# Optimization experiments

Hardware: AMD Instinct MI355X
Metric: run time of the kernel (lower is better)

## Reference

```python
import jax, jax.numpy as jnp
import numpy as np

N_NODES = 100000
N_EDGES = 1200000
D_FEAT = 64


def setup_inputs() -> dict:
    key = jax.random.key(0)
    k1, k2, k3 = jax.random.split(key, 3)
    x = jax.random.normal(k1, (N_NODES, D_FEAT), dtype=jnp.float32)
    edge_index = jax.random.randint(k2, (2, N_EDGES), 0, N_NODES, dtype=jnp.int64)
    edge_weight = jax.random.uniform(k3, (N_EDGES, 1), dtype=jnp.float32)
    return {"x": x, "edge_index": edge_index, "edge_weight": edge_weight}


def reference(x, edge_index, edge_weight):
    # flow = source_to_target: j = edge_index[0] (source), i = edge_index[1] (target)
    src, dst = edge_index[0], edge_index[1]
    # message: x_j  (gather along node_dim=-2)
    msg = x[src]                       # [E, D]
    # aggregate: scatter-'sum' with edge_weight scaling
    msg = msg * edge_weight            # [E, D]
    out = jax.ops.segment_sum(msg, dst, num_segments=N_NODES)  # [N, D]
    # update: identity
    return out
```

## Files before the change

### kernel.cpp

```cpp
#include <hip/hip_runtime.h>
#include <hip/hip_bf16.h>


constexpr int D_FEAT        = 64;
constexpr int BIN_SHIFT     = 7;
constexpr int NODES_PER_BIN = 1 << BIN_SHIFT;
constexpr int NBINS_MAX     = 1024;
constexpr int BIN_CAP       = 2048;
constexpr int EPB           = 4096;
constexpr int OVF_CAP       = 32768;

__device__ __forceinline__ int wave_incl_scan(int v, int lane) {
    #pragma unroll
    for (int d = 1; d < 64; d <<= 1) {
        int t = __shfl_up(v, d);
        if (lane >= d) v += t;
    }
    return v;
}

__global__ __launch_bounds__(512) void mp_partition(
    const int* __restrict__ src, const int* __restrict__ dst,
    const float* __restrict__ w,
    int*  __restrict__ gcnt,
    int2* __restrict__ payload,
    int*  __restrict__ ovf_cnt, int4* __restrict__ ovf,
    int n_edges, int nbins)
{
    __shared__ int cnt[NBINS_MAX];
    __shared__ int start[NBINS_MAX];
    __shared__ int cur[NBINS_MAX];
    __shared__ int gbase[NBINS_MAX];
    __shared__ unsigned short binof[EPB];
    __shared__ int2 sorted[EPB];
    __shared__ int wsum[8];

    const int t    = threadIdx.x;
    const int lane = t & 63;
    const int wid  = t >> 6;
    const int base = blockIdx.x * EPB;
    const int nblk = min(EPB, n_edges - base);

    for (int b = t; b < nbins; b += 512) cnt[b] = 0;
    __syncthreads();

    #pragma unroll
    for (int k = 0; k < EPB / (4 * 512); ++k) {
        const int i4 = (base >> 2) + k * 512 + t;
        if (i4 * 4 < n_edges) {
            const int4 d4 = reinterpret_cast<const int4*>(dst)[i4];
            atomicAdd(&cnt[d4.x >> BIN_SHIFT], 1);
            atomicAdd(&cnt[d4.y >> BIN_SHIFT], 1);
            atomicAdd(&cnt[d4.z >> BIN_SHIFT], 1);
            atomicAdd(&cnt[d4.w >> BIN_SHIFT], 1);
        }
    }
    __syncthreads();

    const int b2 = t * 2;
    const int c0 = (b2     < nbins) ? cnt[b2]     : 0;
    const int c1 = (b2 + 1 < nbins) ? cnt[b2 + 1] : 0;
    const int l  = c0 + c1;
    const int incl = wave_incl_scan(l, lane);
    if (lane == 63) wsum[wid] = incl;
    __syncthreads();
    int woff = 0;
    #pragma unroll
    for (int k = 0; k < 8; ++k) woff += (k < wid) ? wsum[k] : 0;
    const int excl = woff + incl - l;
    if (b2     < nbins) { start[b2]     = excl;      cur[b2]     = excl;      }
    if (b2 + 1 < nbins) { start[b2 + 1] = excl + c0; cur[b2 + 1] = excl + c0; }
    __syncthreads();

    for (int b = t; b < nbins; b += 512) {
        const int c = cnt[b];
        if (c > 0) gbase[b] = atomicAdd(&gcnt[b], c);
    }

    #pragma unroll
    for (int k = 0; k < EPB / (4 * 512); ++k) {
        const int i4 = (base >> 2) + k * 512 + t;
        if (i4 * 4 < n_edges) {
            const int4   d4 = reinterpret_cast<const int4*>(dst)[i4];
            const int4   s4 = reinterpret_cast<const int4*>(src)[i4];
            const float4 w4 = reinterpret_cast<const float4*>(w)[i4];
            const int   dd[4] = {d4.x, d4.y, d4.z, d4.w};
            const int   ss[4] = {s4.x, s4.y, s4.z, s4.w};
            const float ww[4] = {w4.x, w4.y, w4.z, w4.w};
            #pragma unroll
            for (int j = 0; j < 4; ++j) {
                const int b   = dd[j] >> BIN_SHIFT;
                const int low = dd[j] & (NODES_PER_BIN - 1);
                const int p   = atomicAdd(&cur[b], 1);
                sorted[p] = make_int2((low << 20) | ss[j], __float_as_int(ww[j]));
                binof[p]  = (unsigned short)b;
            }
        }
    }
    __syncthreads();

    for (int i = t; i < nblk; i += 512) {
        const int b    = binof[i];
        const int idx  = i - start[b];
        const int gpos = gbase[b] + idx;
        const int2 e   = sorted[i];
        if (gpos < BIN_CAP) {
            payload[(size_t)b * BIN_CAP + gpos] = e;
        } else {
            const int op = atomicAdd(ovf_cnt, 1);
            if (op < OVF_CAP)
                ovf[op] = make_int4((b << BIN_SHIFT) + (e.x >> 20),
                                    e.x & 0xFFFFF, e.y, 0);
        }
    }
}

__global__ __launch_bounds__(512) void mp_bin_gather(
    const float* __restrict__ x,
    const int*  __restrict__ gcnt,
    const int2* __restrict__ payload,
    const int*  __restrict__ ovf_cnt, const int4* __restrict__ ovf,
    float* __restrict__ out, int n_nodes)
{
    __shared__ int2 sedge[BIN_CAP];
    __shared__ int ncnt[NODES_PER_BIN];
    __shared__ int nstart[NODES_PER_BIN + 1];
    __shared__ int ncur[NODES_PER_BIN];

    const int b    = blockIdx.x;
    const int t    = threadIdx.x;
    const int lane = t & 63;
    const int wid  = t >> 6;

    const int m = min(gcnt[b], BIN_CAP);
    const int2* pl = payload + (size_t)b * BIN_CAP;

    for (int i = t; i < NODES_PER_BIN; i += 512) ncnt[i] = 0;
    __syncthreads();
    for (int i = t; i < m; i += 512)
        atomicAdd(&ncnt[pl[i].x >> 20], 1);
    __syncthreads();

    if (t < 64) {
        const int a0 = ncnt[t], a1 = ncnt[64 + t];
        const int s0 = wave_incl_scan(a0, t);
        const int s1 = wave_incl_scan(a1, t);
        const int tot0 = __shfl(s0, 63);
        nstart[t]      = s0 - a0;
        nstart[64 + t] = tot0 + s1 - a1;
        if (t == 63) nstart[128] = tot0 + s1;
    }
    __syncthreads();
    for (int i = t; i < NODES_PER_BIN; i += 512) ncur[i] = nstart[i];
    __syncthreads();

    for (int i = t; i < m; i += 512) {
        const int2 e  = pl[i];
        const int p   = atomicAdd(&ncur[e.x >> 20], 1);
        sedge[p] = e;
    }
    __syncthreads();

    const int novf = *ovf_cnt;

    for (int n = wid; n < NODES_PER_BIN; n += 8) {
        const int node = (b << BIN_SHIFT) + n;
        if (node >= n_nodes) break;
        const int s0 = nstart[n], s1 = nstart[n + 1];
        float a0 = 0.f, a1 = 0.f, a2 = 0.f, a3 = 0.f;
        int e = s0;
        for (; e + 4 <= s1; e += 4) {
            const int2 p0 = sedge[e],     p1 = sedge[e + 1];
            const int2 p2 = sedge[e + 2], p3 = sedge[e + 3];
            a0 = fmaf(x[(size_t)(p0.x & 0xFFFFF) * D_FEAT + lane], __int_as_float(p0.y), a0);
            a1 = fmaf(x[(size_t)(p1.x & 0xFFFFF) * D_FEAT + lane], __int_as_float(p1.y), a1);
            a2 = fmaf(x[(size_t)(p2.x & 0xFFFFF) * D_FEAT + lane], __int_as_float(p2.y), a2);
            a3 = fmaf(x[(size_t)(p3.x & 0xFFFFF) * D_FEAT + lane], __int_as_float(p3.y), a3);
        }
        for (; e < s1; ++e) {
            const int2 p = sedge[e];
            a0 = fmaf(x[(size_t)(p.x & 0xFFFFF) * D_FEAT + lane], __int_as_float(p.y), a0);
        }
        float r = (a0 + a1) + (a2 + a3);
        if (novf > 0) {
            const int lim = min(novf, OVF_CAP);
            for (int j = 0; j < lim; ++j) {
                const int4 o = ovf[j];
                if (o.x == node)
                    r = fmaf(x[(size_t)o.y * D_FEAT + lane], __int_as_float(o.z), r);
            }
        }
        out[(size_t)node * D_FEAT + lane] = r;
    }
}

__global__ __launch_bounds__(256) void mp_scatter_atomic(
    const float* __restrict__ x, const int* __restrict__ src,
    const int* __restrict__ dst, const float* __restrict__ w,
    float* __restrict__ out, int n_edges)
{
    const int gtid = blockIdx.x * blockDim.x + threadIdx.x;
    const int edge = gtid >> 6;
    const int lane = threadIdx.x & 63;
    if (edge >= n_edges) return;
    const int s = src[edge];
    const int d = dst[edge];
    const float ww = w[edge];
    atomicAdd(&out[(size_t)d * D_FEAT + lane], x[(size_t)s * D_FEAT + lane] * ww);
}

extern "C" void kernel_launch(void* const* d_in, const int* in_sizes, int n_in,
                              void* d_out, int out_size, void* d_ws, size_t ws_size,
                              hipStream_t stream)
{
    const float* x          = (const float*)d_in[0];
    const int*   edge_index = (const int*)d_in[1];
    const float* w          = (const float*)d_in[2];
    float*       out        = (float*)d_out;

    const int n_edges = in_sizes[1] / 2;
    const int n_nodes = in_sizes[0] / D_FEAT;
    const int* src = edge_index;
    const int* dst = edge_index + n_edges;

    const int nbins = (n_nodes + NODES_PER_BIN - 1) >> BIN_SHIFT;

    int*  gcnt    = (int*)d_ws;
    int*  ovf_cnt = gcnt + NBINS_MAX;
    int4* ovf     = (int4*)(gcnt + NBINS_MAX + 64);
    int2* payload = (int2*)(ovf + OVF_CAP);
    const size_t need = (size_t)(NBINS_MAX + 64) * 4 + (size_t)OVF_CAP * 16
                      + (size_t)nbins * BIN_CAP * 8;

    const bool ok = (ws_size >= need) && (nbins <= NBINS_MAX) && ((n_edges & 3) == 0);

    if (ok) {
        hipMemsetAsync(gcnt, 0, (size_t)(NBINS_MAX + 64) * 4, stream);
        const int g1 = (n_edges + EPB - 1) / EPB;
        mp_partition<<<g1, 512, 0, stream>>>(src, dst, w, gcnt, payload,
                                             ovf_cnt, ovf, n_edges, nbins);
        mp_bin_gather<<<nbins, 512, 0, stream>>>(x, gcnt, payload,
                                                 ovf_cnt, ovf, out, n_nodes);
        return;
    }

    hipMemsetAsync(d_out, 0, (size_t)out_size * sizeof(float), stream);
    const int grid = (int)(((size_t)n_edges * 64 + 255) / 256);
    mp_scatter_atomic<<<grid, 256, 0, stream>>>(x, src, dst, w, out, n_edges);
}
```

Baseline: 143.1 us.

## Use 1024-thread partition blocks, stage bin edges in LDS, unroll gather by eight

The partition kernel now runs 1024 threads per block, so each thread handles one int4 of edges and one bin, which removes the per-thread loops and keeps the dst load in registers for reuse in the scatter pass. The gather kernel stages the bin payload in a shared-memory buffer so the second counting-sort pass reads LDS instead of global memory. The per-node accumulation loop is unrolled to eight independent accumulators to put more gathers of x in flight. In exchange, gather uses more LDS (an extra 16KB) and more registers, which may lower occupancy.

```diff
diff --git a/kernel.cpp b/kernel.cpp
--- a/kernel.cpp
+++ b/kernel.cpp
@@ -19,7 +19,7 @@
     return v;
 }
 
-__global__ __launch_bounds__(512) void mp_partition(
+__global__ __launch_bounds__(1024) void mp_partition(
     const int* __restrict__ src, const int* __restrict__ dst,
     const float* __restrict__ w,
     int*  __restrict__ gcnt,
@@ -33,7 +33,7 @@
     __shared__ int gbase[NBINS_MAX];
     __shared__ unsigned short binof[EPB];
     __shared__ int2 sorted[EPB];
-    __shared__ int wsum[8];
+    __shared__ int wsum[16];
 
     const int t    = threadIdx.x;
     const int lane = t & 63;
@@ -41,65 +41,57 @@
     const int base = blockIdx.x * EPB;
     const int nblk = min(EPB, n_edges - base);
 
-    for (int b = t; b < nbins; b += 512) cnt[b] = 0;
-    __syncthreads();
-
-    #pragma unroll
-    for (int k = 0; k < EPB / (4 * 512); ++k) {
-        const int i4 = (base >> 2) + k * 512 + t;
-        if (i4 * 4 < n_edges) {
-            const int4 d4 = reinterpret_cast<const int4*>(dst)[i4];
-            atomicAdd(&cnt[d4.x >> BIN_SHIFT], 1);
-            atomicAdd(&cnt[d4.y >> BIN_SHIFT], 1);
-            atomicAdd(&cnt[d4.z >> BIN_SHIFT], 1);
-            atomicAdd(&cnt[d4.w >> BIN_SHIFT], 1);
-        }
-    }
-    __syncthreads();
-
-    const int b2 = t * 2;
-    const int c0 = (b2     < nbins) ? cnt[b2]     : 0;
-    const int c1 = (b2 + 1 < nbins) ? cnt[b2 + 1] : 0;
-    const int l  = c0 + c1;
-    const int incl = wave_incl_scan(l, lane);
+    if (t < NBINS_MAX) cnt[t] = 0;
+    __syncthreads();
+
+    const int i4 = (base >> 2) + t;
+    int4 d4 = make_int4(0, 0, 0, 0);
+    bool have = (i4 * 4 < n_edges);
+    if (have) {
+        d4 = reinterpret_cast<const int4*>(dst)[i4];
+        atomicAdd(&cnt[d4.x >> BIN_SHIFT], 1);
+        atomicAdd(&cnt[d4.y >> BIN_SHIFT], 1);
+        atomicAdd(&cnt[d4.z >> BIN_SHIFT], 1);
+        atomicAdd(&cnt[d4.w >> BIN_SHIFT], 1);
+    }
+    __syncthreads();
+
+    const int c = (t < nbins) ? cnt[t] : 0;
+    const int incl = wave_incl_scan(c, lane);
     if (lane == 63) wsum[wid] = incl;
     __syncthreads();
     int woff = 0;
     #pragma unroll
-    for (int k = 0; k < 8; ++k) woff += (k < wid) ? wsum[k] : 0;
-    const int excl = woff + incl - l;
-    if (b2     < nbins) { start[b2]     = excl;      cur[b2]     = excl;      }
-    if (b2 + 1 < nbins) { start[b2 + 1] = excl + c0; cur[b2 + 1] = excl + c0; }
-    __syncthreads();
-
-    for (int b = t; b < nbins; b += 512) {
-        const int c = cnt[b];
-        if (c > 0) gbase[b] = atomicAdd(&gcnt[b], c);
-    }
+    for (int k = 0; k < 16; ++k) woff += (k < wid) ? wsum[k] : 0;
+    const int excl = woff + incl - c;
+    if (t < nbins) {
+        start[t] = excl;
+        cur[t]   = excl;
+        if (c > 0) gbase[t] = atomicAdd(&gcnt[t], c);
+    }
+    __syncthreads();
+
+    if (have) {
+        const int4   s4 = reinterpret_cast<const int4*>(src)[i4];
+        const float4 w4 = reinterpret_cast<const float4*>(w)[i4];
+        const int   dd[4] = {d4.x, d4.y, d4.z, d4.w};
+        const int   ss[4] = {s4.x, s4.y, s4.z, s4.w};
+        const float ww[4] = {w4.x, w4.y, w4.z, w4.w};
+        #pragma unroll
+        for (int j = 0; j < 4; ++j) {
+            const int b   = dd[j] >> BIN_SHIFT;
+            const int low = dd[j] & (NODES_PER_BIN - 1);
+            const int p   = atomicAdd(&cur[b], 1);
+            sorted[p] = make_int2((low << 20) | ss[j], __float_as_int(ww[j]));
+            binof[p]  = (unsigned short)b;
+        }
+    }
+    __syncthreads();
 
     #pragma unroll
-    for (int k = 0; k < EPB / (4 * 512); ++k) {
-        const int i4 = (base >> 2) + k * 512 + t;
-        if (i4 * 4 < n_edges) {
-            const int4   d4 = reinterpret_cast<const int4*>(dst)[i4];
-            const int4   s4 = reinterpret_cast<const int4*>(src)[i4];
-            const float4 w4 = reinterpret_cast<const float4*>(w)[i4];
-            const int   dd[4] = {d4.x, d4.y, d4.z, d4.w};
-            const int   ss[4] = {s4.x, s4.y, s4.z, s4.w};
-            const float ww[4] = {w4.x, w4.y, w4.z, w4.w};
-            #pragma unroll
-            for (int j = 0; j < 4; ++j) {
-                const int b   = dd[j] >> BIN_SHIFT;
-                const int low = dd[j] & (NODES_PER_BIN - 1);
-                const int p   = atomicAdd(&cur[b], 1);
-                sorted[p] = make_int2((low << 20) | ss[j], __float_as_int(ww[j]));
-                binof[p]  = (unsigned short)b;
-            }
-        }
-    }
-    __syncthreads();
-
-    for (int i = t; i < nblk; i += 512) {
+    for (int k = 0; k < EPB / 1024; ++k) {
+        const int i = k * 1024 + t;
+        if (i >= nblk) break;
         const int b    = binof[i];
         const int idx  = i - start[b];
         const int gpos = gbase[b] + idx;
@@ -122,6 +114,7 @@
     const int*  __restrict__ ovf_cnt, const int4* __restrict__ ovf,
     float* __restrict__ out, int n_nodes)
 {
+    __shared__ int2 sraw[BIN_CAP];
     __shared__ int2 sedge[BIN_CAP];
     __shared__ int ncnt[NODES_PER_BIN];
     __shared__ int nstart[NODES_PER_BIN + 1];
@@ -137,8 +130,12 @@
 
     for (int i = t; i < NODES_PER_BIN; i += 512) ncnt[i] = 0;
     __syncthreads();
-    for (int i = t; i < m; i += 512)
-        atomicAdd(&ncnt[pl[i].x >> 20], 1);
+
+    for (int i = t; i < m; i += 512) {
+        const int2 e = pl[i];
+        sraw[i] = e;
+        atomicAdd(&ncnt[e.x >> 20], 1);
+    }
     __syncthreads();
 
     if (t < 64) {
@@ -155,8 +152,8 @@
     __syncthreads();
 
     for (int i = t; i < m; i += 512) {
-        const int2 e  = pl[i];
-        const int p   = atomicAdd(&ncur[e.x >> 20], 1);
+        const int2 e = sraw[i];
+        const int p  = atomicAdd(&ncur[e.x >> 20], 1);
         sedge[p] = e;
     }
     __syncthreads();
@@ -168,20 +165,36 @@
         if (node >= n_nodes) break;
         const int s0 = nstart[n], s1 = nstart[n + 1];
         float a0 = 0.f, a1 = 0.f, a2 = 0.f, a3 = 0.f;
+        float a4 = 0.f, a5 = 0.f, a6 = 0.f, a7 = 0.f;
         int e = s0;
-        for (; e + 4 <= s1; e += 4) {
+        for (; e + 8 <= s1; e += 8) {
+            const int2 p0 = sedge[e],     p1 = sedge[e + 1];
+            const int2 p2 = sedge[e + 2], p3 = sedge[e + 3];
+            const int2 p4 = sedge[e + 4], p5 = sedge[e + 5];
+            const int2 p6 = sedge[e + 6], p7 = sedge[e + 7];
+            a0 = fmaf(x[(size_t)(p0.x & 0xFFFFF) * D_FEAT + lane], __int_as_float(p0.y), a0);
+            a1 = fmaf(x[(size_t)(p1.x & 0xFFFFF) * D_FEAT + lane], __int_as_float(p1.y), a1);
+            a2 = fmaf(x[(size_t)(p2.x & 0xFFFFF) * D_FEAT + lane], __int_as_float(p2.y), a2);
+            a3 = fmaf(x[(size_t)(p3.x & 0xFFFFF) * D_FEAT + lane], __int_as_float(p3.y), a3);
+            a4 = fmaf(x[(size_t)(p4.x & 0xFFFFF) * D_FEAT + lane], __int_as_float(p4.y), a4);
+            a5 = fmaf(x[(size_t)(p5.x & 0xFFFFF) * D_FEAT + lane], __int_as_float(p5.y), a5);
+            a6 = fmaf(x[(size_t)(p6.x & 0xFFFFF) * D_FEAT + lane], __int_as_float(p6.y), a6);
+            a7 = fmaf(x[(size_t)(p7.x & 0xFFFFF) * D_FEAT + lane], __int_as_float(p7.y), a7);
+        }
+        if (e + 4 <= s1) {
             const int2 p0 = sedge[e],     p1 = sedge[e + 1];
             const int2 p2 = sedge[e + 2], p3 = sedge[e + 3];
             a0 = fmaf(x[(size_t)(p0.x & 0xFFFFF) * D_FEAT + lane], __int_as_float(p0.y), a0);
             a1 = fmaf(x[(size_t)(p1.x & 0xFFFFF) * D_FEAT + lane], __int_as_float(p1.y), a1);
             a2 = fmaf(x[(size_t)(p2.x & 0xFFFFF) * D_FEAT + lane], __int_as_float(p2.y), a2);
             a3 = fmaf(x[(size_t)(p3.x & 0xFFFFF) * D_FEAT + lane], __int_as_float(p3.y), a3);
+            e += 4;
         }
         for (; e < s1; ++e) {
             const int2 p = sedge[e];
             a0 = fmaf(x[(size_t)(p.x & 0xFFFFF) * D_FEAT + lane], __int_as_float(p.y), a0);
         }
-        float r = (a0 + a1) + (a2 + a3);
+        float r = ((a0 + a1) + (a2 + a3)) + ((a4 + a5) + (a6 + a7));
         if (novf > 0) {
             const int lim = min(novf, OVF_CAP);
             for (int j = 0; j < lim; ++j) {
@@ -237,8 +250,8 @@
     if (ok) {
         hipMemsetAsync(gcnt, 0, (size_t)(NBINS_MAX + 64) * 4, stream);
         const int g1 = (n_edges + EPB - 1) / EPB;
-        mp_partition<<<g1, 512, 0, stream>>>(src, dst, w, gcnt, payload,
-                                             ovf_cnt, ovf, n_edges, nbins);
+        mp_partition<<<g1, 1024, 0, stream>>>(src, dst, w, gcnt, payload,
+                                              ovf_cnt, ovf, n_edges, nbins);
         mp_bin_gather<<<nbins, 512, 0, stream>>>(x, gcnt, payload,
                                                  ovf_cnt, ovf, out, n_nodes);
         return;
```

After: 136.8 us. 1.05x faster.
